# Kernel tuning notes

Measured on AMD Instinct MI355X. Metric: run time of the kernel, lower is better.

Reference implementation:

```python
import jax, jax.numpy as jnp
import numpy as np

D = 100  # hard-coded model dim from the source
L, BS = 4096, 64


def setup_inputs() -> dict:
    key = jax.random.key(0)
    k_x, k_w, k_b, k_s = jax.random.split(key, 4)
    x = jax.random.normal(k_x, (L, BS, 1, D), dtype=jnp.float32)
    # nn.Linear(D, D): weight [D, D] (out, in), bias [D]
    lim = 1.0 / np.sqrt(D)
    W = jax.random.uniform(k_w, (D, D), dtype=jnp.float32, minval=-lim, maxval=lim)
    b = jax.random.uniform(k_b, (D,), dtype=jnp.float32, minval=-lim, maxval=lim)
    # self.states ~ Normal(0, 0.02), shape [D, D]
    states = 0.02 * jax.random.normal(k_s, (D, D), dtype=jnp.float32)
    return {"x": x, "W": W, "b": b, "states": states}


def reference(x, W, b, states):
    # z1 = layer1(x): x [L, BS, 1, D] @ W.T + b
    z1 = jnp.einsum("lbod,ed->lboe", x, W) + b
    # scan: carry = tile(states) is constant across steps (f multiplies by 1.0),
    # so output[i] = z1[i] @ states for every timestep -> one fused batched matmul.
    out = jnp.einsum("lbod,de->lboe", z1, states)
    return out
```

## Files before the change

kernel.cpp:

```cpp
#include <hip/hip_runtime.h>

typedef __bf16 bf16x8 __attribute__((ext_vector_type(8)));
typedef float  f32x4  __attribute__((ext_vector_type(4)));

#define D100 100
#define NROWS (4096*64)
#define NTILES (NROWS/16)
#define NCT 7
#define NKS 4
#define FRAG_ELEMS (NCT*NKS*64*8)
#define NBLOCKS 1024
#define WAVES_TOTAL (NBLOCKS*4)

__global__ __launch_bounds__(256) void prep_kernel(
    const float* __restrict__ W, const float* __restrict__ bvec,
    const float* __restrict__ S, __bf16* __restrict__ wsM,
    float* __restrict__ wsc) {
  int tid = blockIdx.x * 256 + threadIdx.x;
  if (tid < FRAG_ELEMS) {
    int j    = tid & 7;
    int lane = (tid >> 3) & 63;
    int ks   = (tid >> 9) & 3;
    int ct   = tid >> 11;
    int k = ks * 32 + ((lane >> 4) * 8) + j;
    int n = ct * 16 + (lane & 15);
    float acc = 0.f;
    if (k < D100 && n < D100) {
      float a0 = 0.f, a1 = 0.f, a2 = 0.f, a3 = 0.f;
      for (int d = 0; d < D100; d += 4) {
        a0 += W[(d + 0) * D100 + k] * S[(d + 0) * D100 + n];
        a1 += W[(d + 1) * D100 + k] * S[(d + 1) * D100 + n];
        a2 += W[(d + 2) * D100 + k] * S[(d + 2) * D100 + n];
        a3 += W[(d + 3) * D100 + k] * S[(d + 3) * D100 + n];
      }
      acc = (a0 + a1) + (a2 + a3);
    }
    wsM[tid] = (__bf16)acc;
  } else if (tid < FRAG_ELEMS + 128) {
    int n = tid - FRAG_ELEMS;
    if (n < D100) {
      float a = 0.f;
      for (int d = 0; d < D100; ++d) a += bvec[d] * S[d * D100 + n];
      wsc[n] = a;
    }
  }
}

__global__ __launch_bounds__(256) void gemm_kernel(
    const float* __restrict__ x, const __bf16* __restrict__ wsM,
    const float* __restrict__ wsc, float* __restrict__ out) {
  const int lane = threadIdx.x & 63;
  const int l16  = lane & 15;
  const int lg   = lane >> 4;
  const int gwave = blockIdx.x * 4 + (threadIdx.x >> 6);

  bf16x8 bfrag[NCT][NKS];
  const bf16x8* wsMv = (const bf16x8*)wsM;
#pragma unroll
  for (int ct = 0; ct < NCT; ++ct)
#pragma unroll
    for (int ks = 0; ks < NKS; ++ks)
      bfrag[ct][ks] = wsMv[(ct * NKS + ks) * 64 + lane];

  float cval[NCT];
#pragma unroll
  for (int ct = 0; ct < NCT; ++ct) {
    int col = ct * 16 + l16;
    cval[ct] = (col < D100) ? wsc[col] : 0.f;
  }

  for (int tile = gwave; tile < NTILES; tile += WAVES_TOTAL) {
    const float* xr = x + (size_t)tile * (16 * D100) + l16 * D100;

    f32x4 acc[NCT];
#pragma unroll
    for (int ct = 0; ct < NCT; ++ct)
      acc[ct] = (f32x4){cval[ct], cval[ct], cval[ct], cval[ct]};

#pragma unroll
    for (int ks = 0; ks < NKS; ++ks) {
      bf16x8 af;
      const int k0 = ks * 32 + lg * 8;
      if (ks < 3) {
        f32x4 v0 = *(const f32x4*)(xr + k0);
        f32x4 v1 = *(const f32x4*)(xr + k0 + 4);
#pragma unroll
        for (int j = 0; j < 4; ++j) {
          af[j]     = (__bf16)v0[j];
          af[j + 4] = (__bf16)v1[j];
        }
      } else {
        f32x4 v0 = {0.f, 0.f, 0.f, 0.f};
        if (lg == 0) v0 = *(const f32x4*)(xr + 96);
#pragma unroll
        for (int j = 0; j < 4; ++j) {
          af[j]     = (__bf16)v0[j];
          af[j + 4] = (__bf16)0.f;
        }
      }
#pragma unroll
      for (int ct = 0; ct < NCT; ++ct)
        acc[ct] = __builtin_amdgcn_mfma_f32_16x16x32_bf16(
            af, bfrag[ct][ks], acc[ct], 0, 0, 0);
    }

    float* orow = out + (size_t)tile * 16 * D100 + (size_t)(lg * 4) * D100;
#pragma unroll
    for (int ct = 0; ct < NCT; ++ct) {
      int col = ct * 16 + l16;
      if (col < D100) {
#pragma unroll
        for (int r = 0; r < 4; ++r) orow[r * D100 + col] = acc[ct][r];
      }
    }
  }
}

extern "C" void kernel_launch(void* const* d_in, const int* in_sizes, int n_in,
                              void* d_out, int out_size, void* d_ws,
                              size_t ws_size, hipStream_t stream) {
  const float* x = (const float*)d_in[0];
  const float* W = (const float*)d_in[1];
  const float* b = (const float*)d_in[2];
  const float* S = (const float*)d_in[3];
  __bf16* wsM = (__bf16*)d_ws;
  float*  wsc = (float*)((char*)d_ws + (size_t)FRAG_ELEMS * 2);
  float*  out = (float*)d_out;

  hipLaunchKernelGGL(prep_kernel, dim3(57), dim3(256), 0, stream,
                     W, b, S, wsM, wsc);
  hipLaunchKernelGGL(gemm_kernel, dim3(NBLOCKS), dim3(256), 0, stream,
                     x, wsM, wsc, out);
}
```

Baseline: 48.12 us.

## Stage weights and output tile through LDS, one tile per wave

Replaces the persistent grid-stride loop with one 16-row tile per wave over 4096 blocks. The folded weight fragments are staged in LDS instead of per-wave registers, the x loads are issued up front, and the output is written through LDS so each block stores its 64x100 region with coalesced 16-byte stores. The aim is to remove the strided scalar global stores and the per-thread register cost of holding the weights. In exchange, every block reloads the weights into LDS, adds two barriers, and uses about 53 KB of LDS, which limits how many blocks fit per CU.

```diff
diff --git a/kernel.cpp b/kernel.cpp
--- a/kernel.cpp
+++ b/kernel.cpp
@@ -9,8 +9,7 @@
 #define NCT 7
 #define NKS 4
 #define FRAG_ELEMS (NCT*NKS*64*8)
-#define NBLOCKS 1024
-#define WAVES_TOTAL (NBLOCKS*4)
+#define NBLK (NTILES/4)
 
 __global__ __launch_bounds__(256) void prep_kernel(
     const float* __restrict__ W, const float* __restrict__ bvec,
@@ -49,18 +48,22 @@
 __global__ __launch_bounds__(256) void gemm_kernel(
     const float* __restrict__ x, const __bf16* __restrict__ wsM,
     const float* __restrict__ wsc, float* __restrict__ out) {
-  const int lane = threadIdx.x & 63;
+  __shared__ __align__(16) __bf16 ldsB[FRAG_ELEMS];
+  __shared__ __align__(16) float  ldsOut[64 * D100];
+
+  const int t    = threadIdx.x;
+  const int lane = t & 63;
   const int l16  = lane & 15;
   const int lg   = lane >> 4;
-  const int gwave = blockIdx.x * 4 + (threadIdx.x >> 6);
+  const int w    = t >> 6;
+  const int tile = blockIdx.x * 4 + w;
 
-  bf16x8 bfrag[NCT][NKS];
-  const bf16x8* wsMv = (const bf16x8*)wsM;
+  {
+    const f32x4* src = (const f32x4*)wsM;
+    f32x4*       dst = (f32x4*)ldsB;
 #pragma unroll
-  for (int ct = 0; ct < NCT; ++ct)
-#pragma unroll
-    for (int ks = 0; ks < NKS; ++ks)
-      bfrag[ct][ks] = wsMv[(ct * NKS + ks) * 64 + lane];
+    for (int i = 0; i < 7; ++i) dst[i * 256 + t] = src[i * 256 + t];
+  }
 
   float cval[NCT];
 #pragma unroll
@@ -69,51 +72,63 @@
     cval[ct] = (col < D100) ? wsc[col] : 0.f;
   }
 
-  for (int tile = gwave; tile < NTILES; tile += WAVES_TOTAL) {
-    const float* xr = x + (size_t)tile * (16 * D100) + l16 * D100;
+  const float* xr = x + (size_t)tile * (16 * D100) + l16 * D100;
+  f32x4 xv[7];
+#pragma unroll
+  for (int ks = 0; ks < 3; ++ks) {
+    xv[ks * 2]     = *(const f32x4*)(xr + ks * 32 + lg * 8);
+    xv[ks * 2 + 1] = *(const f32x4*)(xr + ks * 32 + lg * 8 + 4);
+  }
+  xv[6] = (lg == 0) ? *(const f32x4*)(xr + 96) : (f32x4){0.f, 0.f, 0.f, 0.f};
 
-    f32x4 acc[NCT];
+  __syncthreads();
+
+  f32x4 acc[NCT];
+#pragma unroll
+  for (int ct = 0; ct < NCT; ++ct)
+    acc[ct] = (f32x4){cval[ct], cval[ct], cval[ct], cval[ct]};
+
+  const bf16x8* Bv = (const bf16x8*)ldsB;
+#pragma unroll
+  for (int ks = 0; ks < NKS; ++ks) {
+    bf16x8 af;
+    if (ks < 3) {
+      f32x4 v0 = xv[ks * 2], v1 = xv[ks * 2 + 1];
+#pragma unroll
+      for (int j = 0; j < 4; ++j) {
+        af[j]     = (__bf16)v0[j];
+        af[j + 4] = (__bf16)v1[j];
+      }
+    } else {
+      f32x4 v0 = xv[6];
+#pragma unroll
+      for (int j = 0; j < 4; ++j) {
+        af[j]     = (__bf16)v0[j];
+        af[j + 4] = (__bf16)0.f;
+      }
+    }
 #pragma unroll
     for (int ct = 0; ct < NCT; ++ct)
-      acc[ct] = (f32x4){cval[ct], cval[ct], cval[ct], cval[ct]};
+      acc[ct] = __builtin_amdgcn_mfma_f32_16x16x32_bf16(
+          af, Bv[(ct * NKS + ks) * 64 + lane], acc[ct], 0, 0, 0);
+  }
 
 #pragma unroll
-    for (int ks = 0; ks < NKS; ++ks) {
-      bf16x8 af;
-      const int k0 = ks * 32 + lg * 8;
-      if (ks < 3) {
-        f32x4 v0 = *(const f32x4*)(xr + k0);
-        f32x4 v1 = *(const f32x4*)(xr + k0 + 4);
+  for (int ct = 0; ct < NCT; ++ct) {
+    int col = ct * 16 + l16;
+    if (col < D100) {
 #pragma unroll
-        for (int j = 0; j < 4; ++j) {
-          af[j]     = (__bf16)v0[j];
-          af[j + 4] = (__bf16)v1[j];
-        }
-      } else {
-        f32x4 v0 = {0.f, 0.f, 0.f, 0.f};
-        if (lg == 0) v0 = *(const f32x4*)(xr + 96);
-#pragma unroll
-        for (int j = 0; j < 4; ++j) {
-          af[j]     = (__bf16)v0[j];
-          af[j + 4] = (__bf16)0.f;
-        }
-      }
-#pragma unroll
-      for (int ct = 0; ct < NCT; ++ct)
-        acc[ct] = __builtin_amdgcn_mfma_f32_16x16x32_bf16(
-            af, bfrag[ct][ks], acc[ct], 0, 0, 0);
-    }
-
-    float* orow = out + (size_t)tile * 16 * D100 + (size_t)(lg * 4) * D100;
-#pragma unroll
-    for (int ct = 0; ct < NCT; ++ct) {
-      int col = ct * 16 + l16;
-      if (col < D100) {
-#pragma unroll
-        for (int r = 0; r < 4; ++r) orow[r * D100 + col] = acc[ct][r];
-      }
+      for (int r = 0; r < 4; ++r)
+        ldsOut[(w * 16 + lg * 4 + r) * D100 + col] = acc[ct][r];
     }
   }
+  __syncthreads();
+
+  f32x4*       ob = (f32x4*)(out + (size_t)blockIdx.x * (64 * D100));
+  const f32x4* lo = (const f32x4*)ldsOut;
+#pragma unroll
+  for (int i = 0; i < 6; ++i) ob[i * 256 + t] = lo[i * 256 + t];
+  if (t < 64) ob[1536 + t] = lo[1536 + t];
 }
 
 extern "C" void kernel_launch(void* const* d_in, const int* in_sizes, int n_in,
@@ -129,6 +144,6 @@
 
   hipLaunchKernelGGL(prep_kernel, dim3(57), dim3(256), 0, stream,
                      W, b, S, wsM, wsc);
-  hipLaunchKernelGGL(gemm_kernel, dim3(NBLOCKS), dim3(256), 0, stream,
+  hipLaunchKernelGGL(gemm_kernel, dim3(NBLK), dim3(256), 0, stream,
                      x, wsM, wsc, out);
 }
```

Result: faster. 45.89 us (-4.6%).
